# Kernel optimization log

Measured on AMD Instinct MI355X. Metric: run time of the kernel, lower is better.

The kernel has to match this reference:

```python
import math
import jax, jax.numpy as jnp
import numpy as np

B, L, D, H = 4, 512, 256, 8
DH = D // H
BUCKETS = 11  # rel_pos_buckets; padding_idx = BUCKETS


def setup_inputs() -> dict:
    key = jax.random.key(0)
    ks = jax.random.split(key, 12)
    s = 0.02
    rel_table = jax.random.normal(ks[10], (BUCKETS + 1, D), dtype=jnp.float32) * s
    rel_table = rel_table.at[BUCKETS].set(0.0)  # padding_idx row is zero
    return {
        "inputs": jax.random.normal(ks[0], (B, L, D), dtype=jnp.float32),
        "mask": jax.random.randint(ks[1], (B, L, L), 0, 2) > 0,
        "distances": jax.random.randint(ks[2], (B, L, L), 0, BUCKETS + 1),
        "Wq": jax.random.normal(ks[3], (D, D), dtype=jnp.float32) * s,
        "bq": jnp.zeros((D,), jnp.float32),
        "Wk": jax.random.normal(ks[4], (D, D), dtype=jnp.float32) * s,
        "bk": jnp.zeros((D,), jnp.float32),
        "Wv": jax.random.normal(ks[5], (D, D), dtype=jnp.float32) * s,
        "bv": jnp.zeros((D,), jnp.float32),
        "Wo": jax.random.normal(ks[6], (D, D), dtype=jnp.float32) * s,
        "bo": jnp.zeros((D,), jnp.float32),
        "rel_table": rel_table,
        "u": jax.random.normal(ks[7], (D,), dtype=jnp.float32) * s,
        "v": jax.random.normal(ks[8], (D,), dtype=jnp.float32) * s,
    }


def reference(inputs, mask, distances, Wq, bq, Wk, bk, Wv, bv, Wo, bo, rel_table, u, v):
    def shape(x):  # (B, L, D) -> (B, H, L, DH)
        return x.reshape(B, L, H, DH).transpose(0, 2, 1, 3)

    q = shape(inputs @ Wq + bq) / math.sqrt(DH)
    k = shape(inputs @ Wk + bk)
    val = shape(inputs @ Wv + bv)

    # content term: (q + u) k^T
    a_c = jnp.einsum("bhqd,bhkd->bhqk", q + u.reshape(1, H, 1, DH), k)

    # relative-position term: embedding gather (padding row already zero, mask anyway)
    valid = (distances != BUCKETS)[..., None].astype(rel_table.dtype)
    rel = (rel_table[distances] * valid).reshape(B, L, L, H, DH)  # (B, Lq, Lk, H, DH)
    b_d = jnp.einsum("bhqd,bqkhd->bhqk", q + v.reshape(1, H, 1, DH), rel)

    scores = jnp.where(mask[:, None, :, :], jnp.float32(-1e18), a_c + b_d)
    attn = jax.nn.softmax(scores, axis=-1)  # (B, H, Lq, Lk)

    ctx = jnp.einsum("bhqk,bhkd->bhqd", attn, val)
    ctx = ctx.transpose(0, 2, 1, 3).reshape(B, L, D)
    output = ctx @ Wo + bo
    return output, attn
```

## Files before the change

### kernel.cpp

```cpp
#include <hip/hip_runtime.h>
#include <math.h>

#define BB 4
#define LL 512
#define DD 256
#define HH 8
#define DHH 32
#define NB 12

__global__ __launch_bounds__(256) void qkv_kernel(const float* __restrict__ x,
    const float* __restrict__ Wq, const float* __restrict__ bq,
    const float* __restrict__ Wk, const float* __restrict__ bk,
    const float* __restrict__ Wv, const float* __restrict__ bv,
    const float* __restrict__ uvec, const float* __restrict__ vvec,
    float* __restrict__ Qu, float* __restrict__ Qv,
    float* __restrict__ KT, float* __restrict__ V) {
    __shared__ float xs[8][DD];
    const int mat = blockIdx.x >> 8;
    const int r0 = (blockIdx.x & 255) * 8;
    const int t = threadIdx.x;
    const int cg = t & 63, rg = t >> 6;
    const int c0 = cg * 4;
    {
        const float4* xg = (const float4*)(x + r0 * DD);
        float4* xsv = (float4*)&xs[0][0];
        xsv[t] = xg[t];
        xsv[t + 256] = xg[t + 256];
    }
    __syncthreads();
    const float* W    = (mat == 0) ? Wq : (mat == 1) ? Wk : Wv;
    const float* bias = (mat == 0) ? bq : (mat == 1) ? bk : bv;
    float acc[2][4];
#pragma unroll
    for (int r = 0; r < 2; ++r)
#pragma unroll
        for (int c = 0; c < 4; ++c) acc[r][c] = bias[c0 + c];
    for (int i0 = 0; i0 < DD; i0 += 4) {
        float4 wv4[4], xv4[2];
#pragma unroll
        for (int j = 0; j < 4; ++j) wv4[j] = *(const float4*)&W[(i0 + j) * DD + c0];
#pragma unroll
        for (int r = 0; r < 2; ++r) xv4[r] = *(const float4*)&xs[rg * 2 + r][i0];
        const float* wf = (const float*)wv4;
        const float* xf = (const float*)xv4;
#pragma unroll
        for (int r = 0; r < 2; ++r)
#pragma unroll
            for (int j = 0; j < 4; ++j)
#pragma unroll
                for (int c = 0; c < 4; ++c)
                    acc[r][c] = fmaf(xf[r * 4 + j], wf[j * 4 + c], acc[r][c]);
    }
    if (mat == 0) {
        const float s = 0.17677669529663687f;
        const float4 u4 = *(const float4*)&uvec[c0];
        const float4 v4 = *(const float4*)&vvec[c0];
#pragma unroll
        for (int r = 0; r < 2; ++r) {
            const int row = r0 + rg * 2 + r;
            float4 q = make_float4(acc[r][0] * s, acc[r][1] * s, acc[r][2] * s, acc[r][3] * s);
            *(float4*)&Qu[row * DD + c0] = make_float4(q.x + u4.x, q.y + u4.y, q.z + u4.z, q.w + u4.w);
            *(float4*)&Qv[row * DD + c0] = make_float4(q.x + v4.x, q.y + v4.y, q.z + v4.z, q.w + v4.w);
        }
    } else if (mat == 1) {
        const int b = r0 >> 9;
        const int kb = (r0 & 511) + rg * 2;
#pragma unroll
        for (int c = 0; c < 4; ++c) {
            const int col = c0 + c;
            const int h = col >> 5, dd = col & 31;
            float* p = KT + ((long)((b * HH + h) * DHH + dd)) * LL + kb;
            p[0] = acc[0][c];
            p[1] = acc[1][c];
        }
    } else {
#pragma unroll
        for (int r = 0; r < 2; ++r)
            *(float4*)&V[(r0 + rg * 2 + r) * DD + c0] =
                make_float4(acc[r][0], acc[r][1], acc[r][2], acc[r][3]);
    }
}

__global__ void relp_kernel(const float* __restrict__ Qv, const float* __restrict__ rel_table,
                            float* __restrict__ P) {
    const int idx = blockIdx.x * blockDim.x + threadIdx.x;
    if (idx >= BB * HH * LL * NB) return;
    const int t = idx % NB;
    const int rest = idx / NB;
    const int q = rest % LL;
    const int bh = rest / LL;
    const int h = bh % HH;
    const int b = bh / HH;
    const float* qp = Qv + (b * LL + q) * DD + h * DHH;
    const float* rp = rel_table + t * DD + h * DHH;
    float a = 0.f;
#pragma unroll
    for (int d4 = 0; d4 < DHH; d4 += 4) {
        const float4 qq = *(const float4*)&qp[d4];
        const float4 rr = *(const float4*)&rp[d4];
        a = fmaf(qq.x, rr.x, fmaf(qq.y, rr.y, fmaf(qq.z, rr.z, fmaf(qq.w, rr.w, a))));
    }
    P[idx] = a;
}

__global__ __launch_bounds__(512) void scores_kernel(const float* __restrict__ Qu,
    const float* __restrict__ KT, const float* __restrict__ P,
    const int* __restrict__ mask, const int* __restrict__ dist,
    float* __restrict__ attn) {
    __shared__ float Qs[16][DHH];
    __shared__ float Ps[16][NB];
    const int blk = blockIdx.x;
    const int h = blk & 7;
    const int rest = blk >> 3;
    const int qt = rest & 31;
    const int b = rest >> 5;
    const int q0 = qt * 16;
    const int t = threadIdx.x;
    const int w = t >> 6, l = t & 63;
    {
        const int r = t >> 5, c = t & 31;
        Qs[r][c] = Qu[(b * LL + q0 + r) * DD + h * DHH + c];
    }
    if (t < 16 * NB) {
        Ps[t / NB][t % NB] = P[((b * HH + h) * LL + q0 + t / NB) * NB + t % NB];
    }
    __syncthreads();

    const int r0 = 2 * w;
    const long kbase = (long)(b * HH + h) * DHH * LL;
    float e0[2][4], e1[2][4];
    float sum0 = 0.f, sum1 = 0.f;
#pragma unroll
    for (int s = 0; s < 2; ++s) {
        const int k0 = 4 * l + 256 * s;
        const int4 dx0 = *(const int4*)&dist[(b * LL + q0 + r0) * LL + k0];
        const int4 dx1 = *(const int4*)&dist[(b * LL + q0 + r0 + 1) * LL + k0];
        const int4 mx0 = *(const int4*)&mask[(b * LL + q0 + r0) * LL + k0];
        const int4 mx1 = *(const int4*)&mask[(b * LL + q0 + r0 + 1) * LL + k0];
        float s0[4], s1[4];
        s0[0] = Ps[r0][dx0.x]; s0[1] = Ps[r0][dx0.y]; s0[2] = Ps[r0][dx0.z]; s0[3] = Ps[r0][dx0.w];
        s1[0] = Ps[r0 + 1][dx1.x]; s1[1] = Ps[r0 + 1][dx1.y]; s1[2] = Ps[r0 + 1][dx1.z]; s1[3] = Ps[r0 + 1][dx1.w];
#pragma unroll
        for (int d4 = 0; d4 < DHH; d4 += 4) {
            const float4 q0v = *(const float4*)&Qs[r0][d4];
            const float4 q1v = *(const float4*)&Qs[r0 + 1][d4];
            float4 kv[4];
#pragma unroll
            for (int j = 0; j < 4; ++j)
                kv[j] = *(const float4*)&KT[kbase + (long)(d4 + j) * LL + k0];
            const float* qf0 = (const float*)&q0v;
            const float* qf1 = (const float*)&q1v;
#pragma unroll
            for (int j = 0; j < 4; ++j) {
                s0[0] = fmaf(qf0[j], kv[j].x, s0[0]);
                s0[1] = fmaf(qf0[j], kv[j].y, s0[1]);
                s0[2] = fmaf(qf0[j], kv[j].z, s0[2]);
                s0[3] = fmaf(qf0[j], kv[j].w, s0[3]);
                s1[0] = fmaf(qf1[j], kv[j].x, s1[0]);
                s1[1] = fmaf(qf1[j], kv[j].y, s1[1]);
                s1[2] = fmaf(qf1[j], kv[j].z, s1[2]);
                s1[3] = fmaf(qf1[j], kv[j].w, s1[3]);
            }
        }
        e0[s][0] = mx0.x ? 0.f : __expf(s0[0]);
        e0[s][1] = mx0.y ? 0.f : __expf(s0[1]);
        e0[s][2] = mx0.z ? 0.f : __expf(s0[2]);
        e0[s][3] = mx0.w ? 0.f : __expf(s0[3]);
        e1[s][0] = mx1.x ? 0.f : __expf(s1[0]);
        e1[s][1] = mx1.y ? 0.f : __expf(s1[1]);
        e1[s][2] = mx1.z ? 0.f : __expf(s1[2]);
        e1[s][3] = mx1.w ? 0.f : __expf(s1[3]);
        sum0 += (e0[s][0] + e0[s][1]) + (e0[s][2] + e0[s][3]);
        sum1 += (e1[s][0] + e1[s][1]) + (e1[s][2] + e1[s][3]);
    }
    for (int off = 32; off > 0; off >>= 1) {
        sum0 += __shfl_xor(sum0, off);
        sum1 += __shfl_xor(sum1, off);
    }
    const float i0 = 1.0f / sum0, i1 = 1.0f / sum1;
    float* a0 = attn + ((long)(b * HH + h) * LL + q0 + r0) * LL;
    float* a1 = a0 + LL;
#pragma unroll
    for (int s = 0; s < 2; ++s) {
        const int k0 = 4 * l + 256 * s;
        *(float4*)&a0[k0] = make_float4(e0[s][0] * i0, e0[s][1] * i0, e0[s][2] * i0, e0[s][3] * i0);
        *(float4*)&a1[k0] = make_float4(e1[s][0] * i1, e1[s][1] * i1, e1[s][2] * i1, e1[s][3] * i1);
    }
}

__global__ __launch_bounds__(256) void ctx_out_kernel(const float* __restrict__ attn,
    const float* __restrict__ V, const float* __restrict__ Wo,
    const float* __restrict__ bo, float* __restrict__ out) {
    __shared__ float Cs[4][DD];
    const int blk = blockIdx.x;
    const int b = blk >> 7;
    const int q0 = (blk & 127) * 4;
    const int d = threadIdx.x;
    const int h = d >> 5;
    const float* vb = V + b * LL * DD + d;
    const float* ab = attn + ((long)(b * HH + h) * LL + q0) * LL;
    float acc[4][2] = {{0.f,0.f},{0.f,0.f},{0.f,0.f},{0.f,0.f}};
    float vA[8], vB[8];
    float4 pA[4][2], pB[4][2];
#pragma unroll
    for (int j = 0; j < 8; ++j) vA[j] = vb[j * DD];
#pragma unroll
    for (int q = 0; q < 4; ++q) {
        pA[q][0] = *(const float4*)&ab[q * LL];
        pA[q][1] = *(const float4*)&ab[q * LL + 4];
    }
    for (int k0 = 0; k0 < LL; k0 += 16) {
#pragma unroll
        for (int j = 0; j < 8; ++j) vB[j] = vb[(k0 + 8 + j) * DD];
#pragma unroll
        for (int q = 0; q < 4; ++q) {
            pB[q][0] = *(const float4*)&ab[q * LL + k0 + 8];
            pB[q][1] = *(const float4*)&ab[q * LL + k0 + 12];
        }
#pragma unroll
        for (int q = 0; q < 4; ++q) {
            acc[q][0] = fmaf(pA[q][0].x, vA[0], fmaf(pA[q][0].y, vA[1],
                        fmaf(pA[q][0].z, vA[2], fmaf(pA[q][0].w, vA[3], acc[q][0]))));
            acc[q][1] = fmaf(pA[q][1].x, vA[4], fmaf(pA[q][1].y, vA[5],
                        fmaf(pA[q][1].z, vA[6], fmaf(pA[q][1].w, vA[7], acc[q][1]))));
        }
        if (k0 + 16 < LL) {
#pragma unroll
            for (int j = 0; j < 8; ++j) vA[j] = vb[(k0 + 16 + j) * DD];
#pragma unroll
            for (int q = 0; q < 4; ++q) {
                pA[q][0] = *(const float4*)&ab[q * LL + k0 + 16];
                pA[q][1] = *(const float4*)&ab[q * LL + k0 + 20];
            }
        }
#pragma unroll
        for (int q = 0; q < 4; ++q) {
            acc[q][0] = fmaf(pB[q][0].x, vB[0], fmaf(pB[q][0].y, vB[1],
                        fmaf(pB[q][0].z, vB[2], fmaf(pB[q][0].w, vB[3], acc[q][0]))));
            acc[q][1] = fmaf(pB[q][1].x, vB[4], fmaf(pB[q][1].y, vB[5],
                        fmaf(pB[q][1].z, vB[6], fmaf(pB[q][1].w, vB[7], acc[q][1]))));
        }
    }
#pragma unroll
    for (int q = 0; q < 4; ++q) Cs[q][d] = acc[q][0] + acc[q][1];
    __syncthreads();
    float o[4];
#pragma unroll
    for (int q = 0; q < 4; ++q) o[q] = bo[d];
    for (int i0 = 0; i0 < DD; i0 += 8) {
        float wv[8];
#pragma unroll
        for (int j = 0; j < 8; ++j) wv[j] = Wo[(i0 + j) * DD + d];
#pragma unroll
        for (int q = 0; q < 4; ++q) {
            const float4 cA = *(const float4*)&Cs[q][i0];
            const float4 cB = *(const float4*)&Cs[q][i0 + 4];
            o[q] = fmaf(cA.x, wv[0], fmaf(cA.y, wv[1], fmaf(cA.z, wv[2], fmaf(cA.w, wv[3], o[q]))));
            o[q] = fmaf(cB.x, wv[4], fmaf(cB.y, wv[5], fmaf(cB.z, wv[6], fmaf(cB.w, wv[7], o[q]))));
        }
    }
#pragma unroll
    for (int q = 0; q < 4; ++q) out[(b * LL + q0 + q) * DD + d] = o[q];
}

extern "C" void kernel_launch(void* const* d_in, const int* in_sizes, int n_in,
                              void* d_out, int out_size, void* d_ws, size_t ws_size,
                              hipStream_t stream) {
    const float* x    = (const float*)d_in[0];
    const int* mk     = (const int*)d_in[1];
    const int* dist   = (const int*)d_in[2];
    const float* Wq = (const float*)d_in[3];
    const float* bq = (const float*)d_in[4];
    const float* Wk = (const float*)d_in[5];
    const float* bk = (const float*)d_in[6];
    const float* Wv = (const float*)d_in[7];
    const float* bv = (const float*)d_in[8];
    const float* Wo = (const float*)d_in[9];
    const float* bo = (const float*)d_in[10];
    const float* rel_table = (const float*)d_in[11];
    const float* uvec = (const float*)d_in[12];
    const float* vvec = (const float*)d_in[13];

    float* out  = (float*)d_out;
    float* attn = out + BB * LL * DD;

    float* Qu = (float*)d_ws;
    float* Qv = Qu + BB * LL * DD;
    float* KT = Qv + BB * LL * DD;
    float* V  = KT + BB * LL * DD;
    float* P  = V + BB * LL * DD;

    qkv_kernel<<<3 * 256, 256, 0, stream>>>(x, Wq, bq, Wk, bk, Wv, bv, uvec, vvec,
                                            Qu, Qv, KT, V);
    relp_kernel<<<(BB * HH * LL * NB + 255) / 256, 256, 0, stream>>>(Qv, rel_table, P);
    scores_kernel<<<BB * (LL / 16) * HH, 512, 0, stream>>>(Qu, KT, P, mk, dist, attn);
    ctx_out_kernel<<<BB * (LL / 4), 256, 0, stream>>>(attn, V, Wo, bo, out);
}
```

Before: 191.2 us.

## Fuse rel-pos projection and attn@V into scores kernel, split out projection

Removes the separate relp kernel by computing the per-query relative-position dot products in shared memory inside the scores kernel. The normalized attention rows are also kept in shared memory and multiplied by V in the same block, so the attention matrix is no longer read back from global memory. The output projection becomes its own GEMM-style kernel, and the QKV kernel processes 16 rows per block with float4 K-transpose stores. The cost is a 32KB shared buffer per block, which may lower occupancy, and an extra ctx round trip through global memory.

```diff
diff --git a/kernel.cpp b/kernel.cpp
--- a/kernel.cpp
+++ b/kernel.cpp
@@ -15,36 +15,36 @@
     const float* __restrict__ uvec, const float* __restrict__ vvec,
     float* __restrict__ Qu, float* __restrict__ Qv,
     float* __restrict__ KT, float* __restrict__ V) {
-    __shared__ float xs[8][DD];
-    const int mat = blockIdx.x >> 8;
-    const int r0 = (blockIdx.x & 255) * 8;
+    __shared__ float xs[16][DD];
+    const int mat = blockIdx.x >> 7;
+    const int r0 = (blockIdx.x & 127) * 16;
     const int t = threadIdx.x;
     const int cg = t & 63, rg = t >> 6;
     const int c0 = cg * 4;
     {
         const float4* xg = (const float4*)(x + r0 * DD);
         float4* xsv = (float4*)&xs[0][0];
-        xsv[t] = xg[t];
-        xsv[t + 256] = xg[t + 256];
+#pragma unroll
+        for (int j = 0; j < 4; ++j) xsv[t + j * 256] = xg[t + j * 256];
     }
     __syncthreads();
     const float* W    = (mat == 0) ? Wq : (mat == 1) ? Wk : Wv;
     const float* bias = (mat == 0) ? bq : (mat == 1) ? bk : bv;
-    float acc[2][4];
-#pragma unroll
-    for (int r = 0; r < 2; ++r)
+    float acc[4][4];
+#pragma unroll
+    for (int r = 0; r < 4; ++r)
 #pragma unroll
         for (int c = 0; c < 4; ++c) acc[r][c] = bias[c0 + c];
     for (int i0 = 0; i0 < DD; i0 += 4) {
-        float4 wv4[4], xv4[2];
+        float4 wv4[4], xv4[4];
 #pragma unroll
         for (int j = 0; j < 4; ++j) wv4[j] = *(const float4*)&W[(i0 + j) * DD + c0];
 #pragma unroll
-        for (int r = 0; r < 2; ++r) xv4[r] = *(const float4*)&xs[rg * 2 + r][i0];
+        for (int r = 0; r < 4; ++r) xv4[r] = *(const float4*)&xs[rg * 4 + r][i0];
         const float* wf = (const float*)wv4;
         const float* xf = (const float*)xv4;
 #pragma unroll
-        for (int r = 0; r < 2; ++r)
+        for (int r = 0; r < 4; ++r)
 #pragma unroll
             for (int j = 0; j < 4; ++j)
 #pragma unroll
@@ -56,59 +56,40 @@
         const float4 u4 = *(const float4*)&uvec[c0];
         const float4 v4 = *(const float4*)&vvec[c0];
 #pragma unroll
-        for (int r = 0; r < 2; ++r) {
-            const int row = r0 + rg * 2 + r;
+        for (int r = 0; r < 4; ++r) {
+            const int row = r0 + rg * 4 + r;
             float4 q = make_float4(acc[r][0] * s, acc[r][1] * s, acc[r][2] * s, acc[r][3] * s);
             *(float4*)&Qu[row * DD + c0] = make_float4(q.x + u4.x, q.y + u4.y, q.z + u4.z, q.w + u4.w);
             *(float4*)&Qv[row * DD + c0] = make_float4(q.x + v4.x, q.y + v4.y, q.z + v4.z, q.w + v4.w);
         }
     } else if (mat == 1) {
         const int b = r0 >> 9;
-        const int kb = (r0 & 511) + rg * 2;
+        const int kb = (r0 & 511) + rg * 4;
 #pragma unroll
         for (int c = 0; c < 4; ++c) {
             const int col = c0 + c;
             const int h = col >> 5, dd = col & 31;
-            float* p = KT + ((long)((b * HH + h) * DHH + dd)) * LL + kb;
-            p[0] = acc[0][c];
-            p[1] = acc[1][c];
+            *(float4*)&KT[((long)((b * HH + h) * DHH + dd)) * LL + kb] =
+                make_float4(acc[0][c], acc[1][c], acc[2][c], acc[3][c]);
         }
     } else {
 #pragma unroll
-        for (int r = 0; r < 2; ++r)
-            *(float4*)&V[(r0 + rg * 2 + r) * DD + c0] =
+        for (int r = 0; r < 4; ++r)
+            *(float4*)&V[(r0 + rg * 4 + r) * DD + c0] =
                 make_float4(acc[r][0], acc[r][1], acc[r][2], acc[r][3]);
     }
 }
 
-__global__ void relp_kernel(const float* __restrict__ Qv, const float* __restrict__ rel_table,
-                            float* __restrict__ P) {
-    const int idx = blockIdx.x * blockDim.x + threadIdx.x;
-    if (idx >= BB * HH * LL * NB) return;
-    const int t = idx % NB;
-    const int rest = idx / NB;
-    const int q = rest % LL;
-    const int bh = rest / LL;
-    const int h = bh % HH;
-    const int b = bh / HH;
-    const float* qp = Qv + (b * LL + q) * DD + h * DHH;
-    const float* rp = rel_table + t * DD + h * DHH;
-    float a = 0.f;
-#pragma unroll
-    for (int d4 = 0; d4 < DHH; d4 += 4) {
-        const float4 qq = *(const float4*)&qp[d4];
-        const float4 rr = *(const float4*)&rp[d4];
-        a = fmaf(qq.x, rr.x, fmaf(qq.y, rr.y, fmaf(qq.z, rr.z, fmaf(qq.w, rr.w, a))));
-    }
-    P[idx] = a;
-}
-
-__global__ __launch_bounds__(512) void scores_kernel(const float* __restrict__ Qu,
-    const float* __restrict__ KT, const float* __restrict__ P,
-    const int* __restrict__ mask, const int* __restrict__ dist,
-    float* __restrict__ attn) {
+__global__ __launch_bounds__(512) void scores_ctx_kernel(const float* __restrict__ Qu,
+    const float* __restrict__ Qv, const float* __restrict__ KT,
+    const float* __restrict__ rel_table, const int* __restrict__ mask,
+    const int* __restrict__ dist, const float* __restrict__ V,
+    float* __restrict__ attn, float* __restrict__ ctx) {
     __shared__ float Qs[16][DHH];
+    __shared__ float Qv8[16][DHH];
+    __shared__ float rels[NB][DHH + 1];
     __shared__ float Ps[16][NB];
+    __shared__ float Ss[16][LL];
     const int blk = blockIdx.x;
     const int h = blk & 7;
     const int rest = blk >> 3;
@@ -117,12 +98,22 @@
     const int q0 = qt * 16;
     const int t = threadIdx.x;
     const int w = t >> 6, l = t & 63;
+
     {
         const int r = t >> 5, c = t & 31;
-        Qs[r][c] = Qu[(b * LL + q0 + r) * DD + h * DHH + c];
-    }
+        Qs[r][c]  = Qu[(b * LL + q0 + r) * DD + h * DHH + c];
+        Qv8[r][c] = Qv[(b * LL + q0 + r) * DD + h * DHH + c];
+    }
+    if (t < NB * DHH) {
+        rels[t >> 5][t & 31] = rel_table[(t >> 5) * DD + h * DHH + (t & 31)];
+    }
+    __syncthreads();
     if (t < 16 * NB) {
-        Ps[t / NB][t % NB] = P[((b * HH + h) * LL + q0 + t / NB) * NB + t % NB];
+        const int bk = t >> 4, r = t & 15;
+        float a = 0.f;
+#pragma unroll
+        for (int d = 0; d < DHH; ++d) a = fmaf(Qv8[r][d], rels[bk][d], a);
+        Ps[r][bk] = a;
     }
     __syncthreads();
 
@@ -183,84 +174,84 @@
 #pragma unroll
     for (int s = 0; s < 2; ++s) {
         const int k0 = 4 * l + 256 * s;
-        *(float4*)&a0[k0] = make_float4(e0[s][0] * i0, e0[s][1] * i0, e0[s][2] * i0, e0[s][3] * i0);
-        *(float4*)&a1[k0] = make_float4(e1[s][0] * i1, e1[s][1] * i1, e1[s][2] * i1, e1[s][3] * i1);
-    }
-}
-
-__global__ __launch_bounds__(256) void ctx_out_kernel(const float* __restrict__ attn,
-    const float* __restrict__ V, const float* __restrict__ Wo,
-    const float* __restrict__ bo, float* __restrict__ out) {
-    __shared__ float Cs[4][DD];
-    const int blk = blockIdx.x;
-    const int b = blk >> 7;
-    const int q0 = (blk & 127) * 4;
-    const int d = threadIdx.x;
-    const int h = d >> 5;
-    const float* vb = V + b * LL * DD + d;
-    const float* ab = attn + ((long)(b * HH + h) * LL + q0) * LL;
-    float acc[4][2] = {{0.f,0.f},{0.f,0.f},{0.f,0.f},{0.f,0.f}};
+        const float4 o0 = make_float4(e0[s][0] * i0, e0[s][1] * i0, e0[s][2] * i0, e0[s][3] * i0);
+        const float4 o1 = make_float4(e1[s][0] * i1, e1[s][1] * i1, e1[s][2] * i1, e1[s][3] * i1);
+        *(float4*)&a0[k0] = o0;
+        *(float4*)&a1[k0] = o1;
+        *(float4*)&Ss[r0][k0] = o0;
+        *(float4*)&Ss[r0 + 1][k0] = o1;
+    }
+    __syncthreads();
+
+    const int q = t >> 5;
+    const int d = t & 31;
+    const float* vb = V + (long)(b * LL) * DD + h * DHH + d;
+    float accA = 0.f, accB = 0.f;
     float vA[8], vB[8];
-    float4 pA[4][2], pB[4][2];
+    float4 pA0, pA1, pB0, pB1;
 #pragma unroll
     for (int j = 0; j < 8; ++j) vA[j] = vb[j * DD];
-#pragma unroll
-    for (int q = 0; q < 4; ++q) {
-        pA[q][0] = *(const float4*)&ab[q * LL];
-        pA[q][1] = *(const float4*)&ab[q * LL + 4];
-    }
+    pA0 = *(const float4*)&Ss[q][0];
+    pA1 = *(const float4*)&Ss[q][4];
     for (int k0 = 0; k0 < LL; k0 += 16) {
 #pragma unroll
         for (int j = 0; j < 8; ++j) vB[j] = vb[(k0 + 8 + j) * DD];
-#pragma unroll
-        for (int q = 0; q < 4; ++q) {
-            pB[q][0] = *(const float4*)&ab[q * LL + k0 + 8];
-            pB[q][1] = *(const float4*)&ab[q * LL + k0 + 12];
-        }
-#pragma unroll
-        for (int q = 0; q < 4; ++q) {
-            acc[q][0] = fmaf(pA[q][0].x, vA[0], fmaf(pA[q][0].y, vA[1],
-                        fmaf(pA[q][0].z, vA[2], fmaf(pA[q][0].w, vA[3], acc[q][0]))));
-            acc[q][1] = fmaf(pA[q][1].x, vA[4], fmaf(pA[q][1].y, vA[5],
-                        fmaf(pA[q][1].z, vA[6], fmaf(pA[q][1].w, vA[7], acc[q][1]))));
-        }
+        pB0 = *(const float4*)&Ss[q][k0 + 8];
+        pB1 = *(const float4*)&Ss[q][k0 + 12];
+        accA = fmaf(pA0.x, vA[0], fmaf(pA0.y, vA[1], fmaf(pA0.z, vA[2], fmaf(pA0.w, vA[3], accA))));
+        accB = fmaf(pA1.x, vA[4], fmaf(pA1.y, vA[5], fmaf(pA1.z, vA[6], fmaf(pA1.w, vA[7], accB))));
         if (k0 + 16 < LL) {
 #pragma unroll
             for (int j = 0; j < 8; ++j) vA[j] = vb[(k0 + 16 + j) * DD];
-#pragma unroll
-            for (int q = 0; q < 4; ++q) {
-                pA[q][0] = *(const float4*)&ab[q * LL + k0 + 16];
-                pA[q][1] = *(const float4*)&ab[q * LL + k0 + 20];
-            }
-        }
-#pragma unroll
-        for (int q = 0; q < 4; ++q) {
-            acc[q][0] = fmaf(pB[q][0].x, vB[0], fmaf(pB[q][0].y, vB[1],
-                        fmaf(pB[q][0].z, vB[2], fmaf(pB[q][0].w, vB[3], acc[q][0]))));
-            acc[q][1] = fmaf(pB[q][1].x, vB[4], fmaf(pB[q][1].y, vB[5],
-                        fmaf(pB[q][1].z, vB[6], fmaf(pB[q][1].w, vB[7], acc[q][1]))));
-        }
-    }
-#pragma unroll
-    for (int q = 0; q < 4; ++q) Cs[q][d] = acc[q][0] + acc[q][1];
-    __syncthreads();
-    float o[4];
-#pragma unroll
-    for (int q = 0; q < 4; ++q) o[q] = bo[d];
-    for (int i0 = 0; i0 < DD; i0 += 8) {
-        float wv[8];
-#pragma unroll
-        for (int j = 0; j < 8; ++j) wv[j] = Wo[(i0 + j) * DD + d];
-#pragma unroll
-        for (int q = 0; q < 4; ++q) {
-            const float4 cA = *(const float4*)&Cs[q][i0];
-            const float4 cB = *(const float4*)&Cs[q][i0 + 4];
-            o[q] = fmaf(cA.x, wv[0], fmaf(cA.y, wv[1], fmaf(cA.z, wv[2], fmaf(cA.w, wv[3], o[q]))));
-            o[q] = fmaf(cB.x, wv[4], fmaf(cB.y, wv[5], fmaf(cB.z, wv[6], fmaf(cB.w, wv[7], o[q]))));
-        }
-    }
-#pragma unroll
-    for (int q = 0; q < 4; ++q) out[(b * LL + q0 + q) * DD + d] = o[q];
+            pA0 = *(const float4*)&Ss[q][k0 + 16];
+            pA1 = *(const float4*)&Ss[q][k0 + 20];
+        }
+        accA = fmaf(pB0.x, vB[0], fmaf(pB0.y, vB[1], fmaf(pB0.z, vB[2], fmaf(pB0.w, vB[3], accA))));
+        accB = fmaf(pB1.x, vB[4], fmaf(pB1.y, vB[5], fmaf(pB1.z, vB[6], fmaf(pB1.w, vB[7], accB))));
+    }
+    ctx[(b * LL + q0 + q) * DD + h * DHH + d] = accA + accB;
+}
+
+__global__ __launch_bounds__(256) void outproj_kernel(const float* __restrict__ ctx,
+    const float* __restrict__ Wo, const float* __restrict__ bo,
+    float* __restrict__ out) {
+    __shared__ float xs[8][DD];
+    const int r0 = blockIdx.x * 8;
+    const int t = threadIdx.x;
+    const int cg = t & 63, rg = t >> 6;
+    const int c0 = cg * 4;
+    {
+        const float4* xg = (const float4*)(ctx + r0 * DD);
+        float4* xsv = (float4*)&xs[0][0];
+        xsv[t] = xg[t];
+        xsv[t + 256] = xg[t + 256];
+    }
+    __syncthreads();
+    float acc[2][4];
+#pragma unroll
+    for (int r = 0; r < 2; ++r)
+#pragma unroll
+        for (int c = 0; c < 4; ++c) acc[r][c] = bo[c0 + c];
+    for (int i0 = 0; i0 < DD; i0 += 4) {
+        float4 wv4[4], xv4[2];
+#pragma unroll
+        for (int j = 0; j < 4; ++j) wv4[j] = *(const float4*)&Wo[(i0 + j) * DD + c0];
+#pragma unroll
+        for (int r = 0; r < 2; ++r) xv4[r] = *(const float4*)&xs[rg * 2 + r][i0];
+        const float* wf = (const float*)wv4;
+        const float* xf = (const float*)xv4;
+#pragma unroll
+        for (int r = 0; r < 2; ++r)
+#pragma unroll
+            for (int j = 0; j < 4; ++j)
+#pragma unroll
+                for (int c = 0; c < 4; ++c)
+                    acc[r][c] = fmaf(xf[r * 4 + j], wf[j * 4 + c], acc[r][c]);
+    }
+#pragma unroll
+    for (int r = 0; r < 2; ++r)
+        *(float4*)&out[(r0 + rg * 2 + r) * DD + c0] =
+            make_float4(acc[r][0], acc[r][1], acc[r][2], acc[r][3]);
 }
 
 extern "C" void kernel_launch(void* const* d_in, const int* in_sizes, int n_in,
@@ -288,11 +279,11 @@
     float* Qv = Qu + BB * LL * DD;
     float* KT = Qv + BB * LL * DD;
     float* V  = KT + BB * LL * DD;
-    float* P  = V + BB * LL * DD;
-
-    qkv_kernel<<<3 * 256, 256, 0, stream>>>(x, Wq, bq, Wk, bk, Wv, bv, uvec, vvec,
+    float* C  = V + BB * LL * DD;
+
+    qkv_kernel<<<3 * 128, 256, 0, stream>>>(x, Wq, bq, Wk, bk, Wv, bv, uvec, vvec,
                                             Qu, Qv, KT, V);
-    relp_kernel<<<(BB * HH * LL * NB + 255) / 256, 256, 0, stream>>>(Qv, rel_table, P);
-    scores_kernel<<<BB * (LL / 16) * HH, 512, 0, stream>>>(Qu, KT, P, mk, dist, attn);
-    ctx_out_kernel<<<BB * (LL / 4), 256, 0, stream>>>(attn, V, Wo, bo, out);
-}
+    scores_ctx_kernel<<<BB * (LL / 16) * HH, 512, 0, stream>>>(Qu, Qv, KT, rel_table,
+                                                               mk, dist, V, attn, C);
+    outproj_kernel<<<BB * LL / 8, 256, 0, stream>>>(C, Wo, bo, out);
+}
```

Measured after the change: 212.9 us. 1.11x slower.
